# Performance work log

Hardware: AMD Instinct MI355X
Metric: run time of the kernel (lower is better)

Reference implementation:

```python
import jax, jax.numpy as jnp
import numpy as np

N = 262144          # particles
E = N * 32          # neighbor pairs (edges)


def wendland(q, h):
    # 2D Wendland C2 kernel, q = r/h in [0,1]
    C = 7.0 / (np.pi) / (h * h)
    b = jnp.clip(1.0 - q, 0.0, None)
    return C * (b ** 4) * (1.0 + 4.0 * q)


def setup_inputs() -> dict:
    key = jax.random.key(0)
    k1, k2, k3, k4, k5 = jax.random.split(key, 5)
    area = jax.random.uniform(k1, (N,), jnp.float32) * 0.5 + 0.5
    density = jax.random.uniform(k2, (N,), jnp.float32) * 0.2 + 0.9
    restDensity = jnp.ones((N,), jnp.float32) * 998.0
    velocity = jax.random.normal(k3, (N, 2), jnp.float32)
    radialDistance = jax.random.uniform(k4, (E,), jnp.float32)
    neighbors = jax.random.randint(k5, (2, E), 0, N, jnp.int64)
    return {
        "fluidCoefficient": jnp.float32(0.01),
        "area": area,
        "density": density,
        "restDensity": restDensity,
        "velocity": velocity,
        "radialDistance": radialDistance,
        "neighbors": neighbors,
        "support": jnp.float32(0.02),
    }


def reference(fluidCoefficient, area, density, restDensity, velocity,
              radialDistance, neighbors, support):
    i = neighbors[0]
    j = neighbors[1]
    fac = fluidCoefficient * restDensity[j] * area[j]           # [E]
    rho_i = density[i] * restDensity[i]                          # [E]
    rho_j = density[j] * restDensity[j]                          # [E]
    v_ij = velocity[j] - velocity[i]                             # [E,2]
    k = wendland(radialDistance, support)                        # [E]
    term = (fac / (rho_i + rho_j) * 2.0 * k)[:, None] * v_ij     # [E,2]
    correction = jax.ops.segment_sum(term, i, num_segments=area.shape[0])
    return correction
```

## Files before the change

kernel.cpp:

```cpp
#include <hip/hip_runtime.h>
#include <math.h>

#ifndef M_PI
#define M_PI 3.14159265358979323846
#endif

#define NBLK  1024
#define CHUNK 8192
#define BSZ   512
#define BSH   9
#define NBK   512

__global__ void detect_idx_width(const unsigned* __restrict__ words,
                                 int* __restrict__ flag) {
    if (blockIdx.x == 0 && threadIdx.x == 0) {
        int is64 = 1;
#pragma unroll 1
        for (int k = 1; k < 2048; k += 2) {
            if (words[k] != 0u) { is64 = 0; break; }
        }
        *flag = is64;
    }
}

__global__ __launch_bounds__(256) void precompute_particle(
    const float* __restrict__ fc_p, const float* __restrict__ area,
    const float* __restrict__ density, const float* __restrict__ restDensity,
    const float* __restrict__ velocity, float4* __restrict__ pre, int N)
{
    int p = blockIdx.x * 256 + threadIdx.x;
    if (p >= N) return;
    const float fc = fc_p[0];
    const float rD = restDensity[p];
    const float2 v = ((const float2*)velocity)[p];
    pre[p] = make_float4(fc * rD * area[p], density[p] * rD, v.x, v.y);
}

__global__ __launch_bounds__(256) void pass_count(
    const void* __restrict__ nbr, const int* __restrict__ flag,
    unsigned* __restrict__ table, int E, int chunk, int NBnum)
{
    __shared__ unsigned cnt[NBK];
    for (int t = threadIdx.x; t < NBnum; t += 256) cnt[t] = 0u;
    __syncthreads();
    const int is64 = *flag;
    const long long s = (long long)blockIdx.x * chunk;
    long long e = s + chunk; if (e > E) e = E;
    if (is64) {
        const long long* ni = (const long long*)nbr;
        for (long long idx = s + threadIdx.x; idx < e; idx += 256)
            atomicAdd(&cnt[((int)ni[idx]) >> BSH], 1u);
    } else {
        const int* ni = (const int*)nbr;
        for (long long idx = s + threadIdx.x; idx < e; idx += 256)
            atomicAdd(&cnt[ni[idx] >> BSH], 1u);
    }
    __syncthreads();
    for (int t = threadIdx.x; t < NBnum; t += 256)
        table[(size_t)blockIdx.x * NBnum + t] = cnt[t];
}

__global__ __launch_bounds__(NBLK) void scan_blocks(
    unsigned* __restrict__ table, unsigned* __restrict__ btot, int NBnum)
{
    __shared__ unsigned buf[NBLK];
    const int t = threadIdx.x;
    const int k = blockIdx.x;
    buf[t] = table[(size_t)t * NBnum + k];
    __syncthreads();
    for (int o = 1; o < NBLK; o <<= 1) {
        unsigned v = (t >= o) ? buf[t - o] : 0u;
        __syncthreads();
        buf[t] += v;
        __syncthreads();
    }
    table[(size_t)t * NBnum + k] = (t == 0) ? 0u : buf[t - 1];
    if (t == NBLK - 1) btot[k] = buf[t];
}

__global__ void scan_buckets(const unsigned* __restrict__ btot,
                             unsigned* __restrict__ bstart, int NBnum)
{
    __shared__ unsigned buf[1024];
    const int t = threadIdx.x;
    buf[t] = btot[t];
    __syncthreads();
    for (int o = 1; o < NBnum; o <<= 1) {
        unsigned v = (t >= o) ? buf[t - o] : 0u;
        __syncthreads();
        buf[t] += v;
        __syncthreads();
    }
    bstart[t] = (t == 0) ? 0u : buf[t - 1];
    if (t == NBnum - 1) bstart[NBnum] = buf[t];
}

__global__ __launch_bounds__(256) void pass_scatter(
    const void* __restrict__ nbr, const float* __restrict__ rad,
    const int* __restrict__ flag, const unsigned* __restrict__ table,
    const unsigned* __restrict__ bstart, int2* __restrict__ jq,
    int E, int chunk, int NBnum)
{
    __shared__ int2 buf[CHUNK];
    __shared__ unsigned cur[NBK];
    __shared__ unsigned loff[NBK + 1];
    __shared__ unsigned dst[NBK];

    const int b = blockIdx.x;
    const long long s = (long long)b * chunk;
    long long e = s + chunk; if (e > E) e = E;
    const int n = (int)(e - s);
    if (n <= 0) return;
    const int tid = threadIdx.x;

    for (int k = tid; k < NBnum; k += 256) cur[k] = 0u;
    __syncthreads();

    const int is64 = *flag;
    if (is64) {
        const long long* ni = (const long long*)nbr;
        for (long long idx = s + tid; idx < e; idx += 256)
            atomicAdd(&cur[((int)ni[idx]) >> BSH], 1u);
    } else {
        const int* ni = (const int*)nbr;
        for (long long idx = s + tid; idx < e; idx += 256)
            atomicAdd(&cur[ni[idx] >> BSH], 1u);
    }
    __syncthreads();

    for (int o = 1; o < NBnum; o <<= 1) {
        const int t0 = tid, t1 = tid + 256;
        unsigned v0 = (t0 < NBnum) ? cur[t0] : 0u;
        unsigned m0 = (t0 >= o && t0 < NBnum) ? cur[t0 - o] : 0u;
        unsigned v1 = (t1 < NBnum) ? cur[t1] : 0u;
        unsigned m1 = (t1 >= o && t1 < NBnum) ? cur[t1 - o] : 0u;
        __syncthreads();
        if (t0 < NBnum) cur[t0] = v0 + m0;
        if (t1 < NBnum) cur[t1] = v1 + m1;
        __syncthreads();
    }
    for (int k = tid; k < NBnum; k += 256) {
        loff[k] = k ? cur[k - 1] : 0u;
        dst[k] = bstart[k] + table[(size_t)b * NBnum + k];
    }
    if (tid == 0) loff[NBnum] = (unsigned)n;
    __syncthreads();
    for (int k = tid; k < NBnum; k += 256) cur[k] = loff[k];
    __syncthreads();

    if (is64) {
        const long long* ni = (const long long*)nbr;
        const long long* nj = ni + E;
        for (long long idx = s + tid; idx < e; idx += 256) {
            int i = (int)ni[idx];
            int j = (int)nj[idx];
            float q = rad[idx];
            unsigned pos = atomicAdd(&cur[i >> BSH], 1u);
            buf[pos] = make_int2(j | ((i & (BSZ - 1)) << 22),
                                 __float_as_int(q));
        }
    } else {
        const int* ni = (const int*)nbr;
        const int* nj = ni + E;
        for (long long idx = s + tid; idx < e; idx += 256) {
            int i = ni[idx];
            int j = nj[idx];
            float q = rad[idx];
            unsigned pos = atomicAdd(&cur[i >> BSH], 1u);
            buf[pos] = make_int2(j | ((i & (BSZ - 1)) << 22),
                                 __float_as_int(q));
        }
    }
    __syncthreads();

    for (int t = tid; t < n; t += 256) {
        int lo = 0, hi = NBnum;
        while (hi - lo > 1) {
            int mid = (lo + hi) >> 1;
            if (loff[mid] <= (unsigned)t) lo = mid; else hi = mid;
        }
        jq[dst[lo] + ((unsigned)t - loff[lo])] = buf[t];
    }
}

__global__ __launch_bounds__(256) void pass_reduce(
    const int2* __restrict__ jq, const float4* __restrict__ pre,
    const unsigned* __restrict__ bstart, const float* __restrict__ support_p,
    float2* __restrict__ out, int N)
{
    __shared__ float4 plds[BSZ];
    __shared__ float2 acc[BSZ];
    const int k = blockIdx.x;
    const int base = k << BSH;
    for (int t = threadIdx.x; t < BSZ; t += 256) {
        int p = base + t;
        plds[t] = (p < N) ? pre[p] : make_float4(0.f, 0.f, 0.f, 0.f);
        acc[t] = make_float2(0.f, 0.f);
    }
    __syncthreads();
    const float h = support_p[0];
    const float C = 7.0f / ((float)M_PI * h * h);
    const unsigned s = bstart[k];
    const unsigned e = bstart[k + 1];
    for (unsigned idx = s + threadIdx.x; idx < e; idx += 256) {
        const int2 pk = jq[idx];
        const int j = pk.x & ((1 << 22) - 1);
        const int il = (pk.x >> 22) & (BSZ - 1);
        const float q = __int_as_float(pk.y);
        const float4 pj = pre[j];
        const float4 pi = plds[il];
        const float b = fmaxf(1.0f - q, 0.0f);
        const float b2 = b * b;
        const float w = C * (b2 * b2) * fmaf(4.0f, q, 1.0f);
        const float sc = pj.x * 2.0f * w / (pi.y + pj.y);
        atomicAdd(&acc[il].x, sc * (pj.z - pi.z));
        atomicAdd(&acc[il].y, sc * (pj.w - pi.w));
    }
    __syncthreads();
    for (int t = threadIdx.x; t < BSZ; t += 256) {
        int p = base + t;
        if (p < N) out[p] = acc[t];
    }
}

__global__ __launch_bounds__(256) void xsph_edge_kernel(
    const float* __restrict__ fc_p, const float* __restrict__ area,
    const float* __restrict__ density, const float* __restrict__ restDensity,
    const float* __restrict__ velocity, const float* __restrict__ rad,
    const void* __restrict__ nbr, const float* __restrict__ support_p,
    const int* __restrict__ flag, float* __restrict__ out, int E)
{
    const int is64 = *flag;
    const float fc = fc_p[0];
    const float h = support_p[0];
    const float C = 7.0f / ((float)M_PI * h * h);
    const long long e0 =
        (long long)(blockIdx.x * (long long)blockDim.x + threadIdx.x) * 4;
    if (e0 >= (long long)E) return;
    int ii[4], jj[4];
    if (is64) {
        const long long* ni = (const long long*)nbr;
        const long long* nj = ni + E;
#pragma unroll
        for (int k = 0; k < 4; ++k) { ii[k] = (int)ni[e0 + k]; jj[k] = (int)nj[e0 + k]; }
    } else {
        const int* ni = (const int*)nbr;
        const int* nj = ni + E;
        int4 iv = *(const int4*)(ni + e0);
        int4 jv = *(const int4*)(nj + e0);
        ii[0] = iv.x; ii[1] = iv.y; ii[2] = iv.z; ii[3] = iv.w;
        jj[0] = jv.x; jj[1] = jv.y; jj[2] = jv.z; jj[3] = jv.w;
    }
    float4 qv = *(const float4*)(rad + e0);
    float qq[4] = {qv.x, qv.y, qv.z, qv.w};
#pragma unroll
    for (int k = 0; k < 4; ++k) {
        const int i = ii[k], j = jj[k];
        const float rDi = restDensity[i], rDj = restDensity[j];
        const float fac = fc * rDj * area[j];
        const float rho_i = density[i] * rDi, rho_j = density[j] * rDj;
        const float2 vi = *(const float2*)(velocity + 2 * i);
        const float2 vj = *(const float2*)(velocity + 2 * j);
        const float q = qq[k];
        const float b = fmaxf(1.0f - q, 0.0f);
        const float b2 = b * b;
        const float w = C * (b2 * b2) * fmaf(4.0f, q, 1.0f);
        const float s = fac * 2.0f * w / (rho_i + rho_j);
        unsafeAtomicAdd(&out[2 * i],     s * (vj.x - vi.x));
        unsafeAtomicAdd(&out[2 * i + 1], s * (vj.y - vi.y));
    }
}

extern "C" void kernel_launch(void* const* d_in, const int* in_sizes, int n_in,
                              void* d_out, int out_size, void* d_ws, size_t ws_size,
                              hipStream_t stream) {
    const float* fc          = (const float*)d_in[0];
    const float* area        = (const float*)d_in[1];
    const float* density     = (const float*)d_in[2];
    const float* restDensity = (const float*)d_in[3];
    const float* velocity    = (const float*)d_in[4];
    const float* rad         = (const float*)d_in[5];
    const void*  nbr         = d_in[6];
    const float* support     = (const float*)d_in[7];

    const int N = in_sizes[1];
    const int E = in_sizes[5];
    const int NBnum = (N + BSZ - 1) / BSZ;
    const int chunk = (int)(((long long)E + NBLK - 1) / NBLK);

    char* ws = (char*)d_ws;
    size_t off = 0;
    int* flag = (int*)(ws + off);               off += 16;
    float4* pre = (float4*)(ws + off);          off += (size_t)N * 16;
    unsigned* table = (unsigned*)(ws + off);    off += (size_t)NBLK * NBnum * 4;
    off = (off + 15) & ~(size_t)15;
    unsigned* btot = (unsigned*)(ws + off);     off += (size_t)NBnum * 4;
    off = (off + 15) & ~(size_t)15;
    unsigned* bstart = (unsigned*)(ws + off);   off += (size_t)(NBnum + 1) * 4;
    off = (off + 15) & ~(size_t)15;
    int2* jq = (int2*)(ws + off);               off += (size_t)E * 8;
    const size_t need = off;

    detect_idx_width<<<1, 1, 0, stream>>>((const unsigned*)nbr, flag);

    const bool can_sort =
        (ws_size >= need) && (NBnum <= NBK) && (N <= (1 << 22)) &&
        (chunk <= CHUNK) && (E > 0);

    if (can_sort) {
        precompute_particle<<<(N + 255) / 256, 256, 0, stream>>>(
            fc, area, density, restDensity, velocity, pre, N);
        pass_count<<<NBLK, 256, 0, stream>>>(nbr, flag, table, E, chunk, NBnum);
        scan_blocks<<<NBnum, NBLK, 0, stream>>>(table, btot, NBnum);
        scan_buckets<<<1, NBnum, 0, stream>>>(btot, bstart, NBnum);
        pass_scatter<<<NBLK, 256, 0, stream>>>(nbr, rad, flag, table, bstart,
                                               jq, E, chunk, NBnum);
        pass_reduce<<<NBnum, 256, 0, stream>>>(jq, pre, bstart, support,
                                               (float2*)d_out, N);
    } else {
        hipMemsetAsync(d_out, 0, (size_t)out_size * sizeof(float), stream);
        const int threads = 256;
        const long long nthreads = ((long long)E + 3) / 4;
        const int blocks = (int)((nthreads + threads - 1) / threads);
        xsph_edge_kernel<<<blocks, threads, 0, stream>>>(
            fc, area, density, restDensity, velocity, rad, nbr, support, flag,
            (float*)d_out, E);
    }
}
```

Baseline: 229.0 us.

## Reuse block counts in scatter, rework column scan, double count blocks

The per-block bucket counts from the count pass are now read back in the scatter pass instead of recounting the indices. This removes a second full read of the i-index array and its shared-memory atomics. The cross-block scan is rewritten so each block handles 16 bucket columns with coalesced row reads and writes offsets to a separate toff table. NBLK doubles to 2048 with half-size chunks, and the reduce kernel uses 512 threads per bucket block. The trade-off is a larger workspace for the two tables and more scan-table traffic.

```diff
diff --git a/kernel.cpp b/kernel.cpp
--- a/kernel.cpp
+++ b/kernel.cpp
@@ -5,11 +5,15 @@
 #define M_PI 3.14159265358979323846
 #endif
 
-#define NBLK  1024
-#define CHUNK 8192
+#define NBLK  2048
+#define CHUNK 4096
 #define BSZ   512
 #define BSH   9
 #define NBK   512
+
+#define SCAN_GB   16
+#define SCAN_TH   512
+#define SCAN_ROWS (NBLK / SCAN_TH)
 
 __global__ void detect_idx_width(const unsigned* __restrict__ words,
                                  int* __restrict__ flag) {
@@ -60,22 +64,56 @@
         table[(size_t)blockIdx.x * NBnum + t] = cnt[t];
 }
 
-__global__ __launch_bounds__(NBLK) void scan_blocks(
-    unsigned* __restrict__ table, unsigned* __restrict__ btot, int NBnum)
-{
-    __shared__ unsigned buf[NBLK];
+__global__ __launch_bounds__(SCAN_TH) void scan_blocks(
+    const unsigned* __restrict__ table, unsigned* __restrict__ toff,
+    unsigned* __restrict__ btot, int NBnum)
+{
+    __shared__ unsigned sums[SCAN_TH][SCAN_GB + 1];
     const int t = threadIdx.x;
-    const int k = blockIdx.x;
-    buf[t] = table[(size_t)t * NBnum + k];
-    __syncthreads();
-    for (int o = 1; o < NBLK; o <<= 1) {
-        unsigned v = (t >= o) ? buf[t - o] : 0u;
-        __syncthreads();
-        buf[t] += v;
-        __syncthreads();
-    }
-    table[(size_t)t * NBnum + k] = (t == 0) ? 0u : buf[t - 1];
-    if (t == NBLK - 1) btot[k] = buf[t];
+    const int k0 = blockIdx.x * SCAN_GB;
+    unsigned v[SCAN_ROWS][SCAN_GB];
+    unsigned loc[SCAN_GB];
+#pragma unroll
+    for (int g = 0; g < SCAN_GB; ++g) loc[g] = 0u;
+#pragma unroll
+    for (int r = 0; r < SCAN_ROWS; ++r) {
+        const size_t row = (size_t)(t * SCAN_ROWS + r) * NBnum;
+#pragma unroll
+        for (int g = 0; g < SCAN_GB; ++g) {
+            unsigned x = (k0 + g < NBnum) ? table[row + k0 + g] : 0u;
+            v[r][g] = x;
+            loc[g] += x;
+        }
+    }
+#pragma unroll
+    for (int g = 0; g < SCAN_GB; ++g) sums[t][g] = loc[g];
+    __syncthreads();
+    for (int o = 1; o < SCAN_TH; o <<= 1) {
+        unsigned m[SCAN_GB];
+#pragma unroll
+        for (int g = 0; g < SCAN_GB; ++g) m[g] = (t >= o) ? sums[t - o][g] : 0u;
+        __syncthreads();
+#pragma unroll
+        for (int g = 0; g < SCAN_GB; ++g) sums[t][g] += m[g];
+        __syncthreads();
+    }
+    unsigned pre[SCAN_GB];
+#pragma unroll
+    for (int g = 0; g < SCAN_GB; ++g) pre[g] = t ? sums[t - 1][g] : 0u;
+#pragma unroll
+    for (int r = 0; r < SCAN_ROWS; ++r) {
+        const size_t row = (size_t)(t * SCAN_ROWS + r) * NBnum;
+#pragma unroll
+        for (int g = 0; g < SCAN_GB; ++g) {
+            if (k0 + g < NBnum) toff[row + k0 + g] = pre[g];
+            pre[g] += v[r][g];
+        }
+    }
+    if (t == SCAN_TH - 1) {
+#pragma unroll
+        for (int g = 0; g < SCAN_GB; ++g)
+            if (k0 + g < NBnum) btot[k0 + g] = sums[t][g];
+    }
 }
 
 __global__ void scan_buckets(const unsigned* __restrict__ btot,
@@ -98,12 +136,11 @@
 __global__ __launch_bounds__(256) void pass_scatter(
     const void* __restrict__ nbr, const float* __restrict__ rad,
     const int* __restrict__ flag, const unsigned* __restrict__ table,
-    const unsigned* __restrict__ bstart, int2* __restrict__ jq,
-    int E, int chunk, int NBnum)
+    const unsigned* __restrict__ toff, const unsigned* __restrict__ bstart,
+    int2* __restrict__ jq, int E, int chunk, int NBnum)
 {
     __shared__ int2 buf[CHUNK];
     __shared__ unsigned cur[NBK];
-    __shared__ unsigned loff[NBK + 1];
     __shared__ unsigned dst[NBK];
 
     const int b = blockIdx.x;
@@ -113,18 +150,9 @@
     if (n <= 0) return;
     const int tid = threadIdx.x;
 
-    for (int k = tid; k < NBnum; k += 256) cur[k] = 0u;
-    __syncthreads();
-
-    const int is64 = *flag;
-    if (is64) {
-        const long long* ni = (const long long*)nbr;
-        for (long long idx = s + tid; idx < e; idx += 256)
-            atomicAdd(&cur[((int)ni[idx]) >> BSH], 1u);
-    } else {
-        const int* ni = (const int*)nbr;
-        for (long long idx = s + tid; idx < e; idx += 256)
-            atomicAdd(&cur[ni[idx] >> BSH], 1u);
+    for (int k = tid; k < NBnum; k += 256) {
+        cur[k] = table[(size_t)b * NBnum + k];
+        dst[k] = bstart[k] + toff[(size_t)b * NBnum + k];
     }
     __syncthreads();
 
@@ -139,15 +167,17 @@
         if (t1 < NBnum) cur[t1] = v1 + m1;
         __syncthreads();
     }
-    for (int k = tid; k < NBnum; k += 256) {
-        loff[k] = k ? cur[k - 1] : 0u;
-        dst[k] = bstart[k] + table[(size_t)b * NBnum + k];
-    }
-    if (tid == 0) loff[NBnum] = (unsigned)n;
-    __syncthreads();
-    for (int k = tid; k < NBnum; k += 256) cur[k] = loff[k];
-    __syncthreads();
-
+    {
+        const int t0 = tid, t1 = tid + 256;
+        unsigned x0 = (t0 < NBnum) ? (t0 ? cur[t0 - 1] : 0u) : 0u;
+        unsigned x1 = (t1 < NBnum) ? cur[t1 - 1] : 0u;
+        __syncthreads();
+        if (t0 < NBnum) cur[t0] = x0;
+        if (t1 < NBnum) cur[t1] = x1;
+        __syncthreads();
+    }
+
+    const int is64 = *flag;
     if (is64) {
         const long long* ni = (const long long*)nbr;
         const long long* nj = ni + E;
@@ -174,16 +204,17 @@
     __syncthreads();
 
     for (int t = tid; t < n; t += 256) {
-        int lo = 0, hi = NBnum;
-        while (hi - lo > 1) {
+        int lo = 0, hi = NBnum - 1;
+        while (lo < hi) {
             int mid = (lo + hi) >> 1;
-            if (loff[mid] <= (unsigned)t) lo = mid; else hi = mid;
-        }
-        jq[dst[lo] + ((unsigned)t - loff[lo])] = buf[t];
-    }
-}
-
-__global__ __launch_bounds__(256) void pass_reduce(
+            if (cur[mid] > (unsigned)t) hi = mid; else lo = mid + 1;
+        }
+        unsigned start = lo ? cur[lo - 1] : 0u;
+        jq[dst[lo] + ((unsigned)t - start)] = buf[t];
+    }
+}
+
+__global__ __launch_bounds__(512) void pass_reduce(
     const int2* __restrict__ jq, const float4* __restrict__ pre,
     const unsigned* __restrict__ bstart, const float* __restrict__ support_p,
     float2* __restrict__ out, int N)
@@ -192,7 +223,7 @@
     __shared__ float2 acc[BSZ];
     const int k = blockIdx.x;
     const int base = k << BSH;
-    for (int t = threadIdx.x; t < BSZ; t += 256) {
+    for (int t = threadIdx.x; t < BSZ; t += 512) {
         int p = base + t;
         plds[t] = (p < N) ? pre[p] : make_float4(0.f, 0.f, 0.f, 0.f);
         acc[t] = make_float2(0.f, 0.f);
@@ -202,7 +233,7 @@
     const float C = 7.0f / ((float)M_PI * h * h);
     const unsigned s = bstart[k];
     const unsigned e = bstart[k + 1];
-    for (unsigned idx = s + threadIdx.x; idx < e; idx += 256) {
+    for (unsigned idx = s + threadIdx.x; idx < e; idx += 512) {
         const int2 pk = jq[idx];
         const int j = pk.x & ((1 << 22) - 1);
         const int il = (pk.x >> 22) & (BSZ - 1);
@@ -217,7 +248,7 @@
         atomicAdd(&acc[il].y, sc * (pj.w - pi.w));
     }
     __syncthreads();
-    for (int t = threadIdx.x; t < BSZ; t += 256) {
+    for (int t = threadIdx.x; t < BSZ; t += 512) {
         int p = base + t;
         if (p < N) out[p] = acc[t];
     }
@@ -294,6 +325,8 @@
     float4* pre = (float4*)(ws + off);          off += (size_t)N * 16;
     unsigned* table = (unsigned*)(ws + off);    off += (size_t)NBLK * NBnum * 4;
     off = (off + 15) & ~(size_t)15;
+    unsigned* toff = (unsigned*)(ws + off);     off += (size_t)NBLK * NBnum * 4;
+    off = (off + 15) & ~(size_t)15;
     unsigned* btot = (unsigned*)(ws + off);     off += (size_t)NBnum * 4;
     off = (off + 15) & ~(size_t)15;
     unsigned* bstart = (unsigned*)(ws + off);   off += (size_t)(NBnum + 1) * 4;
@@ -311,11 +344,12 @@
         precompute_particle<<<(N + 255) / 256, 256, 0, stream>>>(
             fc, area, density, restDensity, velocity, pre, N);
         pass_count<<<NBLK, 256, 0, stream>>>(nbr, flag, table, E, chunk, NBnum);
-        scan_blocks<<<NBnum, NBLK, 0, stream>>>(table, btot, NBnum);
+        scan_blocks<<<(NBnum + SCAN_GB - 1) / SCAN_GB, SCAN_TH, 0, stream>>>(
+            table, toff, btot, NBnum);
         scan_buckets<<<1, NBnum, 0, stream>>>(btot, bstart, NBnum);
-        pass_scatter<<<NBLK, 256, 0, stream>>>(nbr, rad, flag, table, bstart,
-                                               jq, E, chunk, NBnum);
-        pass_reduce<<<NBnum, 256, 0, stream>>>(jq, pre, bstart, support,
+        pass_scatter<<<NBLK, 256, 0, stream>>>(nbr, rad, flag, table, toff,
+                                               bstart, jq, E, chunk, NBnum);
+        pass_reduce<<<NBnum, 512, 0, stream>>>(jq, pre, bstart, support,
                                                (float2*)d_out, N);
     } else {
         hipMemsetAsync(d_out, 0, (size_t)out_size * sizeof(float), stream);
```

Measured after the change: 228.0 us. Within noise of the previous version (-0.4%).
